# Optimization experiments

Hardware: AMD Instinct MI355X
Metric: run time of the kernel (lower is better)

Reference implementation:

```python
import jax, jax.numpy as jnp
import numpy as np

DIM = 192
SHIFT = 3
PAD = SHIFT // 2  # 1
EPS = 1e-5


def conv1x1(x, w, b):
    # 1x1x1 Conv3d == channel matmul. x: (B,C,D,H,W), w: (O,C), b: (O,)
    return jnp.einsum('bcdhw,oc->bodhw', x, w) + b[None, :, None, None, None]


def group_norm1(x, w, b):
    # GroupNorm(1, C): normalize over (C,D,H,W) per sample, per-channel affine.
    mu = x.mean(axis=(1, 2, 3, 4), keepdims=True)
    var = x.var(axis=(1, 2, 3, 4), keepdims=True)
    xn = (x - mu) * jax.lax.rsqrt(var + EPS)
    return xn * w[None, :, None, None, None] + b[None, :, None, None, None]


def axial_shift(x, axis):
    # reflect-pad all 3 spatial dims, roll channel-chunks along `axis`, crop back.
    R = x.shape[-1]
    xp = jnp.pad(x, ((0, 0), (0, 0), (PAD, PAD), (PAD, PAD), (PAD, PAD)), mode='reflect')
    chunks = jnp.split(xp, SHIFT, axis=1)
    rolled = [jnp.roll(c, s, axis=axis) for c, s in zip(chunks, range(-PAD, PAD + 1))]
    xc = jnp.concatenate(rolled, axis=1)
    return xc[:, :, PAD:PAD + R, PAD:PAD + R, PAD:PAD + R]


def setup_inputs() -> dict:
    key = jax.random.key(0)
    ks = jax.random.split(key, 16)
    B, C, R = 8, DIM, 32
    x = jax.random.normal(ks[0], (B, C, R, R, R), dtype=jnp.float32)
    wmat = lambda k: jax.random.normal(k, (C, C), dtype=jnp.float32) * 0.05
    vec = lambda k: jax.random.normal(k, (C,), dtype=jnp.float32) * 0.05
    return {
        'x': x,
        'w1': wmat(ks[1]), 'b1': vec(ks[2]),
        'n1w': jnp.ones((C,), jnp.float32), 'n1b': jnp.zeros((C,), jnp.float32),
        'w21': wmat(ks[3]), 'b21': vec(ks[4]),
        'w22': wmat(ks[5]), 'b22': vec(ks[6]),
        'w23': wmat(ks[7]), 'b23': vec(ks[8]),
        'n2w': jnp.ones((C,), jnp.float32), 'n2b': jnp.zeros((C,), jnp.float32),
        'w3': wmat(ks[9]), 'b3': vec(ks[10]),
    }


def reference(x, w1, b1, n1w, n1b, w21, b21, w22, b22, w23, b23, n2w, n2b, w3, b3):
    h = conv1x1(x, w1, b1)
    h = group_norm1(h, n1w, n1b)
    h = jax.nn.gelu(h, approximate=False)
    h = axial_shift(h, axis=3)
    h = conv1x1(h, w22, b22)
    h = axial_shift(h, axis=2)
    h = conv1x1(h, w21, b21)
    h = axial_shift(h, axis=4)
    h = conv1x1(h, w23, b23)
    h = jax.nn.gelu(h, approximate=False)
    h = group_norm1(h, n2w, n2b)
    h = conv1x1(h, w3, b3)
    return h
```

## Files before the change

### kernel.cpp

```cpp
#include <hip/hip_runtime.h>
#include <math.h>

#define NCH 192
#define NB 8
#define SPAT 32768
#define TILES_PER_B 512
#define NBLK1 (NB * TILES_PER_B)
#define TPW 4
#define NBLKP (NB * (TILES_PER_B / TPW))
#define NELEM_PER_B ((size_t)NCH * SPAT)

typedef short s16x8 __attribute__((ext_vector_type(8)));
typedef float f32x4 __attribute__((ext_vector_type(4)));

__device__ __forceinline__ float bf2f(unsigned short h) {
  return __uint_as_float(((unsigned)h) << 16);
}
__device__ __forceinline__ unsigned short f2bf(float f) {
  unsigned u = __float_as_uint(f);
  u += 0x7FFF + ((u >> 16) & 1);
  return (unsigned short)(u >> 16);
}
__device__ __forceinline__ unsigned cvt_pk(float lo, float hi) {
  unsigned r;
  asm("v_cvt_pk_bf16_f32 %0, %1, %2" : "=v"(r) : "v"(lo), "v"(hi));
  return r;
}

__device__ __forceinline__ float gelu_f(float x) {
  float x2 = x * x;
  float z2 = x * fmaf(x2, 0.0713548163f, 1.5957769100f);
  float e = __expf(z2);
  float r = __builtin_amdgcn_rcpf(e + 1.0f);
  return fmaf(-r, x, x);
}

__device__ __forceinline__ int rshift(int i, int c) {
  int j = i - (c - 1);
  j = (j < 0) ? 1 : j;
  j = (j > 31) ? 30 : j;
  return j;
}

__device__ __forceinline__ int lds_off(int c, int p, int u) {
  return (c * 64 + p) * 128 + 16 * (((u >> 3) ^ (p & 7) ^ ((p >> 3) & 7)) & 7) + 2 * (u & 7);
}

__device__ __forceinline__ void bar_lgkm() {
  __builtin_amdgcn_sched_barrier(0);
  asm volatile("s_waitcnt lgkmcnt(0)" ::: "memory");
  __builtin_amdgcn_s_barrier();
  asm volatile("" ::: "memory");
  __builtin_amdgcn_sched_barrier(0);
}
__device__ __forceinline__ void bar_plain() {
  __builtin_amdgcn_sched_barrier(0);
  asm volatile("" ::: "memory");
  __builtin_amdgcn_s_barrier();
  asm volatile("" ::: "memory");
  __builtin_amdgcn_sched_barrier(0);
}

template <int SHIFTW>
__device__ __forceinline__ void do_gemm48(const char* __restrict__ B,
                                          const unsigned short* __restrict__ wm,
                                          int wave, int col, int kg,
                                          f32x4 acc[3][4]) {
  const unsigned short* wp = wm + (wave * 48 + col) * NCH + kg * 8;
  s16x8 afc[3], afn[3];
#pragma unroll
  for (int r = 0; r < 3; ++r) afc[r] = *(const s16x8*)(wp + r * 16 * NCH);
#pragma unroll
  for (int ks = 0; ks < 6; ++ks) {
    if (ks < 5) {
#pragma unroll
      for (int r = 0; r < 3; ++r)
        afn[r] = *(const s16x8*)(wp + (ks + 1) * 32 + r * 16 * NCH);
    }
    int k0 = ks * 32 + kg * 8;
    int c = k0 >> 6, u = k0 & 63;
    s16x8 bf[4];
#pragma unroll
    for (int m = 0; m < 4; ++m) {
      int p = m * 16 + col;
      int ps = SHIFTW ? ((p & 32) | rshift(p & 31, c)) : p;
      bf[m] = *(const s16x8*)(B + lds_off(c, ps, u));
    }
#pragma unroll
    for (int r = 0; r < 3; ++r)
#pragma unroll
      for (int m = 0; m < 4; ++m)
        acc[r][m] = __builtin_amdgcn_mfma_f32_16x16x32_bf16(afc[r], bf[m], acc[r][m], 0, 0, 0);
#pragma unroll
    for (int r = 0; r < 3; ++r) afc[r] = afn[r];
  }
}

template <int AX>
__device__ __forceinline__ void stage_load(const char* __restrict__ ib, int p0, int tid,
                                           s16x8 vr[6]) {
#pragma unroll
  for (int j = 0; j < 6; ++j) {
    const int c = j >> 1;
    int p = (j & 1) * 32 + (tid >> 3);
    int G = tid & 7;
    int pp = p0 + p, sp;
    if (AX == 0) sp = pp;
    else if (AX == 3) { int h = (pp >> 5) & 31; sp = pp + (rshift(h, c) - h) * 32; }
    else            { int d = pp >> 10;       sp = pp + (rshift(d, c) - d) * 1024; }
    vr[j] = *(const s16x8*)(ib + (size_t)sp * 384 + (c * 8 + G) * 16);
  }
}

template <int FUSE>
__device__ __forceinline__ void stage_write(char* __restrict__ B, int tid, const s16x8 vr[6],
                                            const unsigned short* __restrict__ acb) {
#pragma unroll
  for (int j = 0; j < 6; ++j) {
    const int c = j >> 1;
    int p = (j & 1) * 32 + (tid >> 3);
    int G = tid & 7;
    if (FUSE) {
      s16x8 aA = *(const s16x8*)(acb + c * 64 + G * 8);
      s16x8 aC = *(const s16x8*)(acb + NCH + c * 64 + G * 8);
      unsigned w[4];
#pragma unroll
      for (int i = 0; i < 4; ++i) {
        float f0 = gelu_f(fmaf(bf2f((unsigned short)vr[j][2 * i]), bf2f((unsigned short)aA[2 * i]),
                               bf2f((unsigned short)aC[2 * i])));
        float f1 = gelu_f(fmaf(bf2f((unsigned short)vr[j][2 * i + 1]), bf2f((unsigned short)aA[2 * i + 1]),
                               bf2f((unsigned short)aC[2 * i + 1])));
        w[i] = cvt_pk(f0, f1);
      }
      *(uint2*)(B + lds_off(c, p, G * 8)) = make_uint2(w[0], w[1]);
      *(uint2*)(B + lds_off(c, p, G * 8 + 4)) = make_uint2(w[2], w[3]);
    } else {
      *(s16x8*)(B + lds_off(c, p, G * 8)) = vr[j];
    }
  }
}

__device__ __forceinline__ void store_tile(const char* __restrict__ L, char* __restrict__ ob,
                                           int tid) {
  int G = tid & 7;
#pragma unroll
  for (int j = 0; j < 6; ++j) {
    const int c = j >> 1;
    int p = (j & 1) * 32 + (tid >> 3);
    s16x8 v = *(const s16x8*)(L + lds_off(c, p, G * 8));
    *(s16x8*)(ob + (size_t)p * 384 + (c * 8 + G) * 16) = v;
  }
}

__device__ __forceinline__ void stats_reduce(float ssum, float ssq, int wave, int lane,
                                             float* red, float* partials, int blk) {
#pragma unroll
  for (int off = 1; off < 64; off <<= 1) {
    ssum += __shfl_xor(ssum, off, 64);
    ssq += __shfl_xor(ssq, off, 64);
  }
  if (lane == 0) { red[wave * 2] = ssum; red[wave * 2 + 1] = ssq; }
  __syncthreads();
  if (wave == 0 && lane == 0) {
    partials[blk * 2] = red[0] + red[2] + red[4] + red[6];
    partials[blk * 2 + 1] = red[1] + red[3] + red[5] + red[7];
  }
}

__global__ __launch_bounds__(256, 4)
void pass1(const float* __restrict__ x, const unsigned short* __restrict__ w1b,
           const float* __restrict__ b1, unsigned short* __restrict__ out,
           float* __restrict__ partials) {
  __shared__ __align__(16) char B[3 * 64 * 128];
  __shared__ float red[8];
  int blk = blockIdx.x, b = blk >> 9, p0 = (blk & 511) * 64;
  int tid = threadIdx.x, wave = tid >> 6, lane = tid & 63;
  int col = lane & 15, kg = lane >> 4;

  const float* xb = x + (size_t)b * NELEM_PER_B + p0;
  int q = tid & 15;
#pragma unroll
  for (int j = 0; j < 6; ++j) {
    int chp = j * 16 + (tid >> 4);
    int ch0 = 2 * chp;
    int cc = chp >> 5, u0 = ch0 & 63;
    const float* s0 = xb + (size_t)ch0 * SPAT + 4 * q;
    f32x4 a = *(const f32x4*)s0;
    f32x4 c2 = *(const f32x4*)(s0 + SPAT);
#pragma unroll
    for (int i = 0; i < 4; ++i)
      *(unsigned*)(B + lds_off(cc, 4 * q + i, u0)) = cvt_pk(a[i], c2[i]);
  }
  __syncthreads();

  f32x4 acc[3][4] = {};
  do_gemm48<0>(B, w1b, wave, col, kg, acc);

  float ssum = 0.f, ssq = 0.f;
  __syncthreads();
#pragma unroll
  for (int r = 0; r < 3; ++r) {
    int rowb = wave * 48 + r * 16 + kg * 4;
    f32x4 bs = *(const f32x4*)(b1 + rowb);
#pragma unroll
    for (int m = 0; m < 4; ++m) {
      int p = m * 16 + col;
      float v0 = acc[r][m][0] + bs[0], v1 = acc[r][m][1] + bs[1];
      float v2 = acc[r][m][2] + bs[2], v3 = acc[r][m][3] + bs[3];
      ssum += (v0 + v1) + (v2 + v3);
      ssq = fmaf(v0, v0, fmaf(v1, v1, fmaf(v2, v2, fmaf(v3, v3, ssq))));
      uint2 pk; pk.x = cvt_pk(v0, v1); pk.y = cvt_pk(v2, v3);
      *(uint2*)(B + lds_off(rowb >> 6, p, rowb & 63)) = pk;
    }
  }
  __syncthreads();
  store_tile(B, (char*)out + ((size_t)b * SPAT + p0) * 384, tid);
  stats_reduce(ssum, ssq, wave, lane, red, partials, blk);
}

template <int AX, int FUSE, int CHAIN, int EPI2>
__global__ __launch_bounds__(256)
void pipe_pass(const unsigned short* __restrict__ in, const unsigned short* __restrict__ wA,
               const float* __restrict__ bA, const unsigned short* __restrict__ wB,
               const float* __restrict__ bB, unsigned short* __restrict__ out,
               float* __restrict__ partials, const unsigned short* __restrict__ ACbf) {
  __shared__ __align__(16) char buf[2][3 * 64 * 128];
  __shared__ float red[8];
  int blk = blockIdx.x, b = blk / (TILES_PER_B / TPW);
  int ti0 = (blk % (TILES_PER_B / TPW)) * TPW;
  int tid = threadIdx.x, wave = tid >> 6, lane = tid & 63;
  int col = lane & 15, kg = lane >> 4;

  const char* ib = (const char*)in + (size_t)b * SPAT * 384;
  const unsigned short* acb = FUSE ? (ACbf + b * 2 * NCH) : nullptr;
  float ssum = 0.f, ssq = 0.f;

  s16x8 vr[6];
  stage_load<AX>(ib, ti0 * 64, tid, vr);

#pragma unroll
  for (int t = 0; t < TPW; ++t) {
    char* W = buf[t & 1];
    int p0 = (ti0 + t) * 64;

    stage_write<FUSE>(W, tid, vr, acb);
    if (t + 1 < TPW) stage_load<AX>(ib, (ti0 + t + 1) * 64, tid, vr);
    bar_lgkm();

    f32x4 acc[3][4] = {};
    do_gemm48<0>(W, wA, wave, col, kg, acc);
    bar_plain();

    if constexpr (CHAIN) {
#pragma unroll
      for (int r = 0; r < 3; ++r) {
        int rowb = wave * 48 + r * 16 + kg * 4;
        f32x4 bs = *(const f32x4*)(bA + rowb);
#pragma unroll
        for (int m = 0; m < 4; ++m) {
          int p = m * 16 + col;
          uint2 pk;
          pk.x = cvt_pk(acc[r][m][0] + bs[0], acc[r][m][1] + bs[1]);
          pk.y = cvt_pk(acc[r][m][2] + bs[2], acc[r][m][3] + bs[3]);
          *(uint2*)(W + lds_off(rowb >> 6, p, rowb & 63)) = pk;
        }
      }
      bar_lgkm();
#pragma unroll
      for (int r = 0; r < 3; ++r)
#pragma unroll
        for (int m = 0; m < 4; ++m) acc[r][m] = (f32x4){0.f, 0.f, 0.f, 0.f};
      do_gemm48<1>(W, wB, wave, col, kg, acc);
      bar_plain();
    }

    const float* bfin = CHAIN ? bB : bA;
#pragma unroll
    for (int r = 0; r < 3; ++r) {
      int rowb = wave * 48 + r * 16 + kg * 4;
      f32x4 bs = *(const f32x4*)(bfin + rowb);
#pragma unroll
      for (int m = 0; m < 4; ++m) {
        int p = m * 16 + col;
        float v0 = acc[r][m][0] + bs[0], v1 = acc[r][m][1] + bs[1];
        float v2 = acc[r][m][2] + bs[2], v3 = acc[r][m][3] + bs[3];
        if (EPI2) {
          v0 = gelu_f(v0); v1 = gelu_f(v1); v2 = gelu_f(v2); v3 = gelu_f(v3);
          ssum += (v0 + v1) + (v2 + v3);
          ssq = fmaf(v0, v0, fmaf(v1, v1, fmaf(v2, v2, fmaf(v3, v3, ssq))));
        }
        uint2 pk; pk.x = cvt_pk(v0, v1); pk.y = cvt_pk(v2, v3);
        *(uint2*)(W + lds_off(rowb >> 6, p, rowb & 63)) = pk;
      }
    }
    bar_lgkm();
    store_tile(W, (char*)out + ((size_t)b * SPAT + p0) * 384, tid);
  }

  if (EPI2) stats_reduce(ssum, ssq, wave, lane, red, partials, blk);
}

__global__ __launch_bounds__(256)
void pass3(const unsigned short* __restrict__ in, const unsigned short* __restrict__ w3e,
           const float* __restrict__ b3e, float* __restrict__ outf) {
  __shared__ __align__(16) char buf[2][3 * 64 * 128];
  int blk = blockIdx.x, b = blk / (TILES_PER_B / TPW);
  int ti0 = (blk % (TILES_PER_B / TPW)) * TPW;
  int tid = threadIdx.x, wave = tid >> 6, lane = tid & 63;
  int col = lane & 15, kg = lane >> 4;

  const char* ib = (const char*)in + (size_t)b * SPAT * 384;
  const unsigned short* wbase = w3e + (size_t)b * NCH * NCH;
  const float* bb = b3e + b * NCH;

  s16x8 vr[6];
  stage_load<0>(ib, ti0 * 64, tid, vr);

#pragma unroll
  for (int t = 0; t < TPW; ++t) {
    char* W = buf[t & 1];
    int p0 = (ti0 + t) * 64;
    stage_write<0>(W, tid, vr, nullptr);
    if (t + 1 < TPW) stage_load<0>(ib, (ti0 + t + 1) * 64, tid, vr);
    bar_lgkm();

    f32x4 acc[3][4] = {};
    do_gemm48<0>(W, wbase, wave, col, kg, acc);
    bar_lgkm();

#pragma unroll
    for (int r = 0; r < 3; ++r) {
      int rowb = wave * 48 + r * 16 + kg * 4;
      f32x4 bs = *(const f32x4*)(bb + rowb);
#pragma unroll
      for (int m = 0; m < 4; ++m) {
        int p = p0 + m * 16 + col;
#pragma unroll
        for (int j = 0; j < 4; ++j)
          outf[((size_t)b * NCH + rowb + j) * SPAT + p] = acc[r][m][j] + bs[j];
      }
    }
  }
}

__global__ void stats_finalize(const float* __restrict__ partials,
                               const float* __restrict__ nw, const float* __restrict__ nb,
                               float* __restrict__ AC, unsigned short* __restrict__ ACbf,
                               int nper) {
  int b = blockIdx.x, tid = threadIdx.x;
  __shared__ float s0[256], s1[256];
  float a = 0.f, c = 0.f;
  for (int i = tid; i < nper; i += 256) {
    a += partials[(b * nper + i) * 2];
    c += partials[(b * nper + i) * 2 + 1];
  }
  s0[tid] = a; s1[tid] = c;
  __syncthreads();
  for (int st = 128; st > 0; st >>= 1) {
    if (tid < st) { s0[tid] += s0[tid + st]; s1[tid] += s1[tid + st]; }
    __syncthreads();
  }
  float inv_n = 1.0f / (float)NELEM_PER_B;
  float mu = s0[0] * inv_n;
  float var = s1[0] * inv_n - mu * mu;
  float rs = rsqrtf(var + 1e-5f);
  if (tid < NCH) {
    float A = rs * nw[tid];
    float C = nb[tid] - mu * A;
    AC[b * 2 * NCH + tid] = A;
    AC[b * 2 * NCH + NCH + tid] = C;
    ACbf[b * 2 * NCH + tid] = f2bf(A);
    ACbf[b * 2 * NCH + NCH + tid] = f2bf(C);
  }
}

__global__ void prep_weights(const float* __restrict__ w1, const float* __restrict__ w21,
                             const float* __restrict__ w22, const float* __restrict__ w23,
                             unsigned short* __restrict__ wb) {
  int i = blockIdx.x * 256 + threadIdx.x;
  if (i >= 4 * NCH * NCH) return;
  int m = i / (NCH * NCH), r = i % (NCH * NCH);
  const float* src = (m == 0) ? w1 : (m == 1) ? w22 : (m == 2) ? w21 : w23;
  wb[i] = f2bf(src[r]);
}

__global__ void prep_w3(const float* __restrict__ w3, const float* __restrict__ b3,
                        const float* __restrict__ AC2,
                        unsigned short* __restrict__ w3e, float* __restrict__ b3e) {
  int b = blockIdx.x, o = threadIdx.x;
  if (o >= NCH) return;
  const float* A = AC2 + b * 2 * NCH;
  const float* C = A + NCH;
  float s = b3[o];
  for (int c = 0; c < NCH; ++c) {
    float w = w3[o * NCH + c];
    w3e[((size_t)b * NCH + o) * NCH + c] = f2bf(w * A[c]);
    s = fmaf(w, C[c], s);
  }
  b3e[b * NCH + o] = s;
}

extern "C" void kernel_launch(void* const* d_in, const int* in_sizes, int n_in,
                              void* d_out, int out_size, void* d_ws, size_t ws_size,
                              hipStream_t stream) {
  const float* x   = (const float*)d_in[0];
  const float* w1  = (const float*)d_in[1];
  const float* b1  = (const float*)d_in[2];
  const float* n1w = (const float*)d_in[3];
  const float* n1b = (const float*)d_in[4];
  const float* w21 = (const float*)d_in[5];
  const float* b21 = (const float*)d_in[6];
  const float* w22 = (const float*)d_in[7];
  const float* b22 = (const float*)d_in[8];
  const float* w23 = (const float*)d_in[9];
  const float* b23 = (const float*)d_in[10];
  const float* n2w = (const float*)d_in[11];
  const float* n2b = (const float*)d_in[12];
  const float* w3  = (const float*)d_in[13];
  const float* b3  = (const float*)d_in[14];

  char* ws = (char*)d_ws;
  size_t off = 0;
  unsigned short* wb = (unsigned short*)(ws + off); off += (size_t)4 * NCH * NCH * 2;
  off = (off + 255) & ~(size_t)255;
  unsigned short* w3e = (unsigned short*)(ws + off); off += (size_t)NB * NCH * NCH * 2;
  off = (off + 255) & ~(size_t)255;
  float* b3e = (float*)(ws + off); off += NB * NCH * 4;
  float* AC1 = (float*)(ws + off); off += NB * 2 * NCH * 4;
  float* AC2 = (float*)(ws + off); off += NB * 2 * NCH * 4;
  unsigned short* ACbf1 = (unsigned short*)(ws + off); off += NB * 2 * NCH * 2;
  unsigned short* ACbf2 = (unsigned short*)(ws + off); off += NB * 2 * NCH * 2;
  off = (off + 255) & ~(size_t)255;
  float* part1 = (float*)(ws + off); off += (size_t)NBLK1 * 2 * 4;
  float* part2 = (float*)(ws + off); off += (size_t)NBLKP * 2 * 4;
  off = (off + 255) & ~(size_t)255;
  unsigned short* R1 = (unsigned short*)(ws + off);
  unsigned short* R2 = (unsigned short*)d_out;

  prep_weights<<<(4 * NCH * NCH + 255) / 256, 256, 0, stream>>>(w1, w21, w22, w23, wb);

  pass1<<<NBLK1, 256, 0, stream>>>(x, wb + 0 * NCH * NCH, b1, R1, part1);
  stats_finalize<<<NB, 256, 0, stream>>>(part1, n1w, n1b, AC1, ACbf1, TILES_PER_B);

  pipe_pass<3, 1, 0, 0><<<NBLKP, 256, 0, stream>>>(
      R1, wb + 1 * NCH * NCH, b22, nullptr, nullptr, R2, nullptr, ACbf1);

  pipe_pass<2, 0, 1, 1><<<NBLKP, 256, 0, stream>>>(
      R2, wb + 2 * NCH * NCH, b21, wb + 3 * NCH * NCH, b23, R1, part2, nullptr);
  stats_finalize<<<NB, 256, 0, stream>>>(part2, n2w, n2b, AC2, ACbf2, TILES_PER_B / TPW);
  prep_w3<<<NB, NCH, 0, stream>>>(w3, b3, AC2, w3e, b3e);

  pass3<<<NBLKP, 256, 0, stream>>>(R1, w3e, b3e, (float*)d_out);
}
```

Baseline: 343.4 us.

## Use 6-wave blocks with register-resident weights and single LDS buffer in pipe kernels

The three pipelined GEMM passes move from 4 waves each computing 48 output rows to 6 waves of 384 threads each computing 32 rows. Each wave now holds its full weight slice in registers, and a single LDS buffer replaces the double buffer, with extra barriers added. Staging and store loops are re-indexed for 384 threads. prep_w3 is parallelized to one 64-lane block per output row with a shuffle reduction. The aim is higher occupancy and more waves to hide latency, at the cost of more register pressure and less overlap from the dropped double buffering.

Result: slower. 576.5 us (+67.9%).

```diff
diff --git a/kernel.cpp b/kernel.cpp
--- a/kernel.cpp
+++ b/kernel.cpp
@@ -61,7 +61,6 @@
   __builtin_amdgcn_sched_barrier(0);
 }
 
-template <int SHIFTW>
 __device__ __forceinline__ void do_gemm48(const char* __restrict__ B,
                                           const unsigned short* __restrict__ wm,
                                           int wave, int col, int kg,
@@ -81,67 +80,108 @@
     int c = k0 >> 6, u = k0 & 63;
     s16x8 bf[4];
 #pragma unroll
+    for (int m = 0; m < 4; ++m)
+      bf[m] = *(const s16x8*)(B + lds_off(c, m * 16 + col, u));
+#pragma unroll
+    for (int r = 0; r < 3; ++r)
+#pragma unroll
+      for (int m = 0; m < 4; ++m)
+        acc[r][m] = __builtin_amdgcn_mfma_f32_16x16x32_bf16(afc[r], bf[m], acc[r][m], 0, 0, 0);
+#pragma unroll
+    for (int r = 0; r < 3; ++r) afc[r] = afn[r];
+  }
+}
+
+__device__ __forceinline__ void load_af32(const unsigned short* __restrict__ wm,
+                                          int wave, int col, int kg, s16x8 af[2][6]) {
+#pragma unroll
+  for (int r = 0; r < 2; ++r)
+#pragma unroll
+    for (int ks = 0; ks < 6; ++ks)
+      af[r][ks] = *(const s16x8*)(wm + (wave * 32 + r * 16 + col) * NCH + ks * 32 + kg * 8);
+}
+
+template <int SHIFTW>
+__device__ __forceinline__ void gemm32(const char* __restrict__ B, const s16x8 af[2][6],
+                                       int col, int kg, f32x4 acc[2][4]) {
+#pragma unroll
+  for (int ks = 0; ks < 6; ++ks) {
+    int k0 = ks * 32 + kg * 8;
+    int c = k0 >> 6, u = k0 & 63;
+    s16x8 bf[4];
+#pragma unroll
     for (int m = 0; m < 4; ++m) {
       int p = m * 16 + col;
       int ps = SHIFTW ? ((p & 32) | rshift(p & 31, c)) : p;
       bf[m] = *(const s16x8*)(B + lds_off(c, ps, u));
     }
 #pragma unroll
-    for (int r = 0; r < 3; ++r)
+    for (int r = 0; r < 2; ++r)
 #pragma unroll
       for (int m = 0; m < 4; ++m)
-        acc[r][m] = __builtin_amdgcn_mfma_f32_16x16x32_bf16(afc[r], bf[m], acc[r][m], 0, 0, 0);
-#pragma unroll
-    for (int r = 0; r < 3; ++r) afc[r] = afn[r];
+        acc[r][m] = __builtin_amdgcn_mfma_f32_16x16x32_bf16(af[r][ks], bf[m], acc[r][m], 0, 0, 0);
   }
 }
 
 template <int AX>
-__device__ __forceinline__ void stage_load(const char* __restrict__ ib, int p0, int tid,
-                                           s16x8 vr[6]) {
-#pragma unroll
-  for (int j = 0; j < 6; ++j) {
-    const int c = j >> 1;
-    int p = (j & 1) * 32 + (tid >> 3);
-    int G = tid & 7;
-    int pp = p0 + p, sp;
-    if (AX == 0) sp = pp;
-    else if (AX == 3) { int h = (pp >> 5) & 31; sp = pp + (rshift(h, c) - h) * 32; }
-    else            { int d = pp >> 10;       sp = pp + (rshift(d, c) - d) * 1024; }
-    vr[j] = *(const s16x8*)(ib + (size_t)sp * 384 + (c * 8 + G) * 16);
+__device__ __forceinline__ void stage_load6(const char* __restrict__ ib, int p0, int tid,
+                                            s16x8 vr[4]) {
+#pragma unroll
+  for (int j = 0; j < 4; ++j) {
+    int g = j * 384 + tid;
+    int p = g / 24, r24 = g - 24 * p;
+    int c = r24 >> 3;
+    int pp = p0 + p, sp = pp;
+    if (AX == 3) { int h = (pp >> 5) & 31; sp = pp + (rshift(h, c) - h) * 32; }
+    if (AX == 2) { int d = pp >> 10;       sp = pp + (rshift(d, c) - d) * 1024; }
+    vr[j] = *(const s16x8*)(ib + (size_t)sp * 384 + r24 * 16);
   }
 }
 
 template <int FUSE>
-__device__ __forceinline__ void stage_write(char* __restrict__ B, int tid, const s16x8 vr[6],
-                                            const unsigned short* __restrict__ acb) {
-#pragma unroll
-  for (int j = 0; j < 6; ++j) {
-    const int c = j >> 1;
-    int p = (j & 1) * 32 + (tid >> 3);
-    int G = tid & 7;
+__device__ __forceinline__ void stage_write6(char* __restrict__ B, int tid, const s16x8 vr[4],
+                                             const unsigned short* __restrict__ acb) {
+#pragma unroll
+  for (int j = 0; j < 4; ++j) {
+    int g = j * 384 + tid;
+    int p = g / 24, r24 = g - 24 * p;
+    int c = r24 >> 3, gr = r24 & 7;
     if (FUSE) {
-      s16x8 aA = *(const s16x8*)(acb + c * 64 + G * 8);
-      s16x8 aC = *(const s16x8*)(acb + NCH + c * 64 + G * 8);
+      int ch0 = r24 * 8;
+      s16x8 aA = *(const s16x8*)(acb + ch0);
+      s16x8 aC = *(const s16x8*)(acb + NCH + ch0);
       unsigned w[4];
 #pragma unroll
       for (int i = 0; i < 4; ++i) {
-        float f0 = gelu_f(fmaf(bf2f((unsigned short)vr[j][2 * i]), bf2f((unsigned short)aA[2 * i]),
+        float f0 = gelu_f(fmaf(bf2f((unsigned short)vr[j][2 * i]),
+                               bf2f((unsigned short)aA[2 * i]),
                                bf2f((unsigned short)aC[2 * i])));
-        float f1 = gelu_f(fmaf(bf2f((unsigned short)vr[j][2 * i + 1]), bf2f((unsigned short)aA[2 * i + 1]),
+        float f1 = gelu_f(fmaf(bf2f((unsigned short)vr[j][2 * i + 1]),
+                               bf2f((unsigned short)aA[2 * i + 1]),
                                bf2f((unsigned short)aC[2 * i + 1])));
         w[i] = cvt_pk(f0, f1);
       }
-      *(uint2*)(B + lds_off(c, p, G * 8)) = make_uint2(w[0], w[1]);
-      *(uint2*)(B + lds_off(c, p, G * 8 + 4)) = make_uint2(w[2], w[3]);
+      *(uint2*)(B + lds_off(c, p, gr * 8)) = make_uint2(w[0], w[1]);
+      *(uint2*)(B + lds_off(c, p, gr * 8 + 4)) = make_uint2(w[2], w[3]);
     } else {
-      *(s16x8*)(B + lds_off(c, p, G * 8)) = vr[j];
-    }
-  }
-}
-
-__device__ __forceinline__ void store_tile(const char* __restrict__ L, char* __restrict__ ob,
-                                           int tid) {
+      *(s16x8*)(B + lds_off(c, p, gr * 8)) = vr[j];
+    }
+  }
+}
+
+__device__ __forceinline__ void store_tile6(const char* __restrict__ L, char* __restrict__ ob,
+                                            int tid) {
+#pragma unroll
+  for (int j = 0; j < 4; ++j) {
+    int g = j * 384 + tid;
+    int p = g / 24, r24 = g - 24 * p;
+    s16x8 v = *(const s16x8*)(L + lds_off(r24 >> 3, p, (r24 & 7) * 8));
+    *(s16x8*)(ob + (size_t)g * 16) = v;
+  }
+}
+
+__device__ __forceinline__ void store_tile4(const char* __restrict__ L, char* __restrict__ ob,
+                                            int tid) {
   int G = tid & 7;
 #pragma unroll
   for (int j = 0; j < 6; ++j) {
@@ -152,6 +192,7 @@
   }
 }
 
+template <int NW>
 __device__ __forceinline__ void stats_reduce(float ssum, float ssq, int wave, int lane,
                                              float* red, float* partials, int blk) {
 #pragma unroll
@@ -162,8 +203,11 @@
   if (lane == 0) { red[wave * 2] = ssum; red[wave * 2 + 1] = ssq; }
   __syncthreads();
   if (wave == 0 && lane == 0) {
-    partials[blk * 2] = red[0] + red[2] + red[4] + red[6];
-    partials[blk * 2 + 1] = red[1] + red[3] + red[5] + red[7];
+    float a = 0.f, c = 0.f;
+#pragma unroll
+    for (int w = 0; w < NW; ++w) { a += red[w * 2]; c += red[w * 2 + 1]; }
+    partials[blk * 2] = a;
+    partials[blk * 2 + 1] = c;
   }
 }
 
@@ -194,7 +238,7 @@
   __syncthreads();
 
   f32x4 acc[3][4] = {};
-  do_gemm48<0>(B, w1b, wave, col, kg, acc);
+  do_gemm48(B, w1b, wave, col, kg, acc);
 
   float ssum = 0.f, ssq = 0.f;
   __syncthreads();
@@ -214,123 +258,167 @@
     }
   }
   __syncthreads();
-  store_tile(B, (char*)out + ((size_t)b * SPAT + p0) * 384, tid);
-  stats_reduce(ssum, ssq, wave, lane, red, partials, blk);
-}
-
-template <int AX, int FUSE, int CHAIN, int EPI2>
-__global__ __launch_bounds__(256)
-void pipe_pass(const unsigned short* __restrict__ in, const unsigned short* __restrict__ wA,
-               const float* __restrict__ bA, const unsigned short* __restrict__ wB,
-               const float* __restrict__ bB, unsigned short* __restrict__ out,
-               float* __restrict__ partials, const unsigned short* __restrict__ ACbf) {
-  __shared__ __align__(16) char buf[2][3 * 64 * 128];
-  __shared__ float red[8];
-  int blk = blockIdx.x, b = blk / (TILES_PER_B / TPW);
-  int ti0 = (blk % (TILES_PER_B / TPW)) * TPW;
-  int tid = threadIdx.x, wave = tid >> 6, lane = tid & 63;
+  store_tile4(B, (char*)out + ((size_t)b * SPAT + p0) * 384, tid);
+  stats_reduce<4>(ssum, ssq, wave, lane, red, partials, blk);
+}
+
+__global__ __launch_bounds__(384, 4)
+void pipe2a(const unsigned short* __restrict__ in, const unsigned short* __restrict__ w22b,
+            const float* __restrict__ b22, unsigned short* __restrict__ out,
+            const unsigned short* __restrict__ ACbf) {
+  __shared__ __align__(16) char B[3 * 64 * 128];
+  int blk = blockIdx.x, b = blk >> 7;
+  int ti0 = (blk & 127) * TPW;
+  int tid = threadIdx.x, wave = tid / 64, lane = tid & 63;
   int col = lane & 15, kg = lane >> 4;
 
   const char* ib = (const char*)in + (size_t)b * SPAT * 384;
-  const unsigned short* acb = FUSE ? (ACbf + b * 2 * NCH) : nullptr;
-  float ssum = 0.f, ssq = 0.f;
-
-  s16x8 vr[6];
-  stage_load<AX>(ib, ti0 * 64, tid, vr);
+  const unsigned short* acb = ACbf + b * 2 * NCH;
+
+  s16x8 vr[4];
+  stage_load6<3>(ib, ti0 * 64, tid, vr);
 
 #pragma unroll
   for (int t = 0; t < TPW; ++t) {
-    char* W = buf[t & 1];
     int p0 = (ti0 + t) * 64;
-
-    stage_write<FUSE>(W, tid, vr, acb);
-    if (t + 1 < TPW) stage_load<AX>(ib, (ti0 + t + 1) * 64, tid, vr);
+    if (t) bar_plain();
+    stage_write6<1>(B, tid, vr, acb);
+    s16x8 af[2][6];
+    load_af32(w22b, wave, col, kg, af);
+    __builtin_amdgcn_sched_barrier(0);
+    if (t + 1 < TPW) stage_load6<3>(ib, (ti0 + t + 1) * 64, tid, vr);
+    __builtin_amdgcn_sched_barrier(0);
     bar_lgkm();
 
-    f32x4 acc[3][4] = {};
-    do_gemm48<0>(W, wA, wave, col, kg, acc);
+    f32x4 acc[2][4] = {};
+    gemm32<0>(B, af, col, kg, acc);
     bar_plain();
-
-    if constexpr (CHAIN) {
-#pragma unroll
-      for (int r = 0; r < 3; ++r) {
-        int rowb = wave * 48 + r * 16 + kg * 4;
-        f32x4 bs = *(const f32x4*)(bA + rowb);
-#pragma unroll
-        for (int m = 0; m < 4; ++m) {
-          int p = m * 16 + col;
-          uint2 pk;
-          pk.x = cvt_pk(acc[r][m][0] + bs[0], acc[r][m][1] + bs[1]);
-          pk.y = cvt_pk(acc[r][m][2] + bs[2], acc[r][m][3] + bs[3]);
-          *(uint2*)(W + lds_off(rowb >> 6, p, rowb & 63)) = pk;
-        }
-      }
-      bar_lgkm();
-#pragma unroll
-      for (int r = 0; r < 3; ++r)
-#pragma unroll
-        for (int m = 0; m < 4; ++m) acc[r][m] = (f32x4){0.f, 0.f, 0.f, 0.f};
-      do_gemm48<1>(W, wB, wave, col, kg, acc);
-      bar_plain();
-    }
-
-    const float* bfin = CHAIN ? bB : bA;
-#pragma unroll
-    for (int r = 0; r < 3; ++r) {
-      int rowb = wave * 48 + r * 16 + kg * 4;
-      f32x4 bs = *(const f32x4*)(bfin + rowb);
+#pragma unroll
+    for (int r = 0; r < 2; ++r) {
+      int rowb = wave * 32 + r * 16 + kg * 4;
+      f32x4 bs = *(const f32x4*)(b22 + rowb);
 #pragma unroll
       for (int m = 0; m < 4; ++m) {
         int p = m * 16 + col;
-        float v0 = acc[r][m][0] + bs[0], v1 = acc[r][m][1] + bs[1];
-        float v2 = acc[r][m][2] + bs[2], v3 = acc[r][m][3] + bs[3];
-        if (EPI2) {
-          v0 = gelu_f(v0); v1 = gelu_f(v1); v2 = gelu_f(v2); v3 = gelu_f(v3);
-          ssum += (v0 + v1) + (v2 + v3);
-          ssq = fmaf(v0, v0, fmaf(v1, v1, fmaf(v2, v2, fmaf(v3, v3, ssq))));
-        }
+        uint2 pk;
+        pk.x = cvt_pk(acc[r][m][0] + bs[0], acc[r][m][1] + bs[1]);
+        pk.y = cvt_pk(acc[r][m][2] + bs[2], acc[r][m][3] + bs[3]);
+        *(uint2*)(B + lds_off(rowb >> 6, p, rowb & 63)) = pk;
+      }
+    }
+    bar_lgkm();
+    store_tile6(B, (char*)out + ((size_t)b * SPAT + p0) * 384, tid);
+  }
+}
+
+__global__ __launch_bounds__(384, 4)
+void pipe2bc(const unsigned short* __restrict__ in, const unsigned short* __restrict__ w21b,
+             const float* __restrict__ b21, const unsigned short* __restrict__ w23b,
+             const float* __restrict__ b23, unsigned short* __restrict__ out,
+             float* __restrict__ partials) {
+  __shared__ __align__(16) char B[3 * 64 * 128];
+  __shared__ float red[12];
+  int blk = blockIdx.x, b = blk >> 7;
+  int ti0 = (blk & 127) * TPW;
+  int tid = threadIdx.x, wave = tid / 64, lane = tid & 63;
+  int col = lane & 15, kg = lane >> 4;
+
+  const char* ib = (const char*)in + (size_t)b * SPAT * 384;
+  float ssum = 0.f, ssq = 0.f;
+
+  s16x8 vr[4];
+  stage_load6<2>(ib, ti0 * 64, tid, vr);
+
+#pragma unroll
+  for (int t = 0; t < TPW; ++t) {
+    int p0 = (ti0 + t) * 64;
+    if (t) bar_plain();
+    stage_write6<0>(B, tid, vr, nullptr);
+    s16x8 af[2][6];
+    load_af32(w21b, wave, col, kg, af);
+    __builtin_amdgcn_sched_barrier(0);
+    if (t + 1 < TPW) stage_load6<2>(ib, (ti0 + t + 1) * 64, tid, vr);
+    __builtin_amdgcn_sched_barrier(0);
+    bar_lgkm();
+
+    f32x4 acc[2][4] = {};
+    gemm32<0>(B, af, col, kg, acc);
+    bar_plain();
+#pragma unroll
+    for (int r = 0; r < 2; ++r) {
+      int rowb = wave * 32 + r * 16 + kg * 4;
+      f32x4 bs = *(const f32x4*)(b21 + rowb);
+#pragma unroll
+      for (int m = 0; m < 4; ++m) {
+        int p = m * 16 + col;
+        uint2 pk;
+        pk.x = cvt_pk(acc[r][m][0] + bs[0], acc[r][m][1] + bs[1]);
+        pk.y = cvt_pk(acc[r][m][2] + bs[2], acc[r][m][3] + bs[3]);
+        *(uint2*)(B + lds_off(rowb >> 6, p, rowb & 63)) = pk;
+      }
+    }
+    load_af32(w23b, wave, col, kg, af);
+    bar_lgkm();
+#pragma unroll
+    for (int r = 0; r < 2; ++r)
+#pragma unroll
+      for (int m = 0; m < 4; ++m) acc[r][m] = (f32x4){0.f, 0.f, 0.f, 0.f};
+    gemm32<1>(B, af, col, kg, acc);
+    bar_plain();
+#pragma unroll
+    for (int r = 0; r < 2; ++r) {
+      int rowb = wave * 32 + r * 16 + kg * 4;
+      f32x4 bs = *(const f32x4*)(b23 + rowb);
+#pragma unroll
+      for (int m = 0; m < 4; ++m) {
+        int p = m * 16 + col;
+        float v0 = gelu_f(acc[r][m][0] + bs[0]), v1 = gelu_f(acc[r][m][1] + bs[1]);
+        float v2 = gelu_f(acc[r][m][2] + bs[2]), v3 = gelu_f(acc[r][m][3] + bs[3]);
+        ssum += (v0 + v1) + (v2 + v3);
+        ssq = fmaf(v0, v0, fmaf(v1, v1, fmaf(v2, v2, fmaf(v3, v3, ssq))));
         uint2 pk; pk.x = cvt_pk(v0, v1); pk.y = cvt_pk(v2, v3);
-        *(uint2*)(W + lds_off(rowb >> 6, p, rowb & 63)) = pk;
+        *(uint2*)(B + lds_off(rowb >> 6, p, rowb & 63)) = pk;
       }
     }
     bar_lgkm();
-    store_tile(W, (char*)out + ((size_t)b * SPAT + p0) * 384, tid);
-  }
-
-  if (EPI2) stats_reduce(ssum, ssq, wave, lane, red, partials, blk);
-}
-
-__global__ __launch_bounds__(256)
-void pass3(const unsigned short* __restrict__ in, const unsigned short* __restrict__ w3e,
+    store_tile6(B, (char*)out + ((size_t)b * SPAT + p0) * 384, tid);
+  }
+  stats_reduce<6>(ssum, ssq, wave, lane, red, partials, blk);
+}
+
+__global__ __launch_bounds__(384, 4)
+void pipe3(const unsigned short* __restrict__ in, const unsigned short* __restrict__ w3e,
            const float* __restrict__ b3e, float* __restrict__ outf) {
-  __shared__ __align__(16) char buf[2][3 * 64 * 128];
-  int blk = blockIdx.x, b = blk / (TILES_PER_B / TPW);
-  int ti0 = (blk % (TILES_PER_B / TPW)) * TPW;
-  int tid = threadIdx.x, wave = tid >> 6, lane = tid & 63;
+  __shared__ __align__(16) char B[3 * 64 * 128];
+  int blk = blockIdx.x, b = blk >> 7;
+  int ti0 = (blk & 127) * TPW;
+  int tid = threadIdx.x, wave = tid / 64, lane = tid & 63;
   int col = lane & 15, kg = lane >> 4;
 
   const char* ib = (const char*)in + (size_t)b * SPAT * 384;
   const unsigned short* wbase = w3e + (size_t)b * NCH * NCH;
   const float* bb = b3e + b * NCH;
 
-  s16x8 vr[6];
-  stage_load<0>(ib, ti0 * 64, tid, vr);
+  s16x8 vr[4];
+  stage_load6<0>(ib, ti0 * 64, tid, vr);
 
 #pragma unroll
   for (int t = 0; t < TPW; ++t) {
-    char* W = buf[t & 1];
     int p0 = (ti0 + t) * 64;
-    stage_write<0>(W, tid, vr, nullptr);
-    if (t + 1 < TPW) stage_load<0>(ib, (ti0 + t + 1) * 64, tid, vr);
+    if (t) bar_plain();
+    stage_write6<0>(B, tid, vr, nullptr);
+    s16x8 af[2][6];
+    load_af32(wbase, wave, col, kg, af);
+    __builtin_amdgcn_sched_barrier(0);
+    if (t + 1 < TPW) stage_load6<0>(ib, (ti0 + t + 1) * 64, tid, vr);
+    __builtin_amdgcn_sched_barrier(0);
     bar_lgkm();
 
-    f32x4 acc[3][4] = {};
-    do_gemm48<0>(W, wbase, wave, col, kg, acc);
-    bar_lgkm();
-
-#pragma unroll
-    for (int r = 0; r < 3; ++r) {
-      int rowb = wave * 48 + r * 16 + kg * 4;
+    f32x4 acc[2][4] = {};
+    gemm32<0>(B, af, col, kg, acc);
+#pragma unroll
+    for (int r = 0; r < 2; ++r) {
+      int rowb = wave * 32 + r * 16 + kg * 4;
       f32x4 bs = *(const f32x4*)(bb + rowb);
 #pragma unroll
       for (int m = 0; m < 4; ++m) {
@@ -384,20 +472,25 @@
   wb[i] = f2bf(src[r]);
 }
 
-__global__ void prep_w3(const float* __restrict__ w3, const float* __restrict__ b3,
-                        const float* __restrict__ AC2,
-                        unsigned short* __restrict__ w3e, float* __restrict__ b3e) {
-  int b = blockIdx.x, o = threadIdx.x;
-  if (o >= NCH) return;
+__global__ void prep_w3p(const float* __restrict__ w3, const float* __restrict__ b3,
+                         const float* __restrict__ AC2,
+                         unsigned short* __restrict__ w3e, float* __restrict__ b3e) {
+  int gb = blockIdx.x;
+  int b = gb / NCH, o = gb - b * NCH;
   const float* A = AC2 + b * 2 * NCH;
   const float* C = A + NCH;
-  float s = b3[o];
-  for (int c = 0; c < NCH; ++c) {
+  int lane = threadIdx.x;
+  float s = 0.f;
+#pragma unroll
+  for (int k = 0; k < 3; ++k) {
+    int c = k * 64 + lane;
     float w = w3[o * NCH + c];
     w3e[((size_t)b * NCH + o) * NCH + c] = f2bf(w * A[c]);
     s = fmaf(w, C[c], s);
   }
-  b3e[b * NCH + o] = s;
+#pragma unroll
+  for (int off = 1; off < 64; off <<= 1) s += __shfl_xor(s, off, 64);
+  if (lane == 0) b3e[b * NCH + o] = b3[o] + s;
 }
 
 extern "C" void kernel_launch(void* const* d_in, const int* in_sizes, int n_in,
@@ -442,13 +535,12 @@
   pass1<<<NBLK1, 256, 0, stream>>>(x, wb + 0 * NCH * NCH, b1, R1, part1);
   stats_finalize<<<NB, 256, 0, stream>>>(part1, n1w, n1b, AC1, ACbf1, TILES_PER_B);
 
-  pipe_pass<3, 1, 0, 0><<<NBLKP, 256, 0, stream>>>(
-      R1, wb + 1 * NCH * NCH, b22, nullptr, nullptr, R2, nullptr, ACbf1);
-
-  pipe_pass<2, 0, 1, 1><<<NBLKP, 256, 0, stream>>>(
-      R2, wb + 2 * NCH * NCH, b21, wb + 3 * NCH * NCH, b23, R1, part2, nullptr);
+  pipe2a<<<NBLKP, 384, 0, stream>>>(R1, wb + 1 * NCH * NCH, b22, R2, ACbf1);
+
+  pipe2bc<<<NBLKP, 384, 0, stream>>>(R2, wb + 2 * NCH * NCH, b21,
+                                     wb + 3 * NCH * NCH, b23, R1, part2);
   stats_finalize<<<NB, 256, 0, stream>>>(part2, n2w, n2b, AC2, ACbf2, TILES_PER_B / TPW);
-  prep_w3<<<NB, NCH, 0, stream>>>(w3, b3, AC2, w3e, b3e);
-
-  pass3<<<NBLKP, 256, 0, stream>>>(R1, w3e, b3e, (float*)d_out);
-}
+  prep_w3p<<<NB * NCH, 64, 0, stream>>>(w3, b3, AC2, w3e, b3e);
+
+  pipe3<<<NBLKP, 384, 0, stream>>>(R1, w3e, b3e, (float*)d_out);
+}
```
